# Performance work log

Measured on AMD Instinct MI355X. Metric: run time of the kernel, lower is better.

## Reference

```python
import jax, jax.numpy as jnp
import numpy as np

ALPHA = 0.2
B, D, C = 512, 128, 64


def setup_inputs() -> dict:
    key = jax.random.key(0)
    k1, k2, k3 = jax.random.split(key, 3)
    x = jax.random.normal(k1, (B, D), dtype=jnp.float32)
    x = x / jnp.linalg.norm(x, axis=-1, keepdims=True)  # unit embeddings (2-2*cos distance)
    target = jax.random.randint(k2, (B,), 0, C)
    # uniform noise used for parallel random choice among semi-hard candidates
    noise = jax.random.uniform(k3, (B, B, B), dtype=jnp.float32)
    return {"output": x, "target": target, "noise": noise}


def reference(output, target, noise):
    # pairwise squared euclidean distance for unit-norm embeddings
    d = 2.0 - 2.0 * (output @ output.T)  # [B, B]
    n = d.shape[0]
    same = target[:, None] == target[None, :]          # [B, B] same-label mask
    neg = ~same                                        # [a, n] valid negatives
    pair_mask = same & ~jnp.eye(n, dtype=bool)         # valid (anchor, positive), a != p
    # L[a, p, nn] = d[a, p] - d[a, nn] + alpha
    L = d[:, :, None] - d[:, None, :] + ALPHA          # [B, B, B]
    cand = (L > 0.0) & (L < ALPHA) & neg[:, None, :]   # semi-hard candidate mask
    has_cand = cand.any(axis=-1)                       # [B, B]
    valid = pair_mask & has_cand
    # random choice among candidates: argmax of uniform noise over masked set
    score = jnp.where(cand, noise, -1.0)
    n_idx = jnp.argmax(score, axis=-1)                 # [B, B] chosen negative per pair
    tl = jnp.take_along_axis(L, n_idx[:, :, None], axis=-1)[..., 0]  # triplet loss per pair
    return jnp.where(valid, jnp.maximum(tl, 0.0), 0.0).sum()
```

## Files before the change

### kernel.cpp

```cpp
#include <hip/hip_runtime.h>

#define NB 512
#define ND 128
#define TALPHA 0.2f

__global__ __launch_bounds__(512) void triplet_mine_kernel(
    const float* __restrict__ x,
    const int*   __restrict__ target,
    const float* __restrict__ noise,
    float*       __restrict__ partial)
{
    const int a    = blockIdx.x;
    const int tid  = threadIdx.x;
    const int lane = tid & 63;
    const int wv   = tid >> 6;

    __shared__ __align__(16) float d_row[NB];
    __shared__ __align__(16) int   tgt[NB];
    __shared__ int   plist[NB];
    __shared__ int   pcnt_w[8];
    __shared__ float wacc_s[8];

    const int t_mine = target[tid];
    const int ta     = target[a];
    tgt[tid] = t_mine;

    const bool m = (t_mine == ta) && (tid != a);
    const unsigned long long b = __ballot(m);
    if (lane == 0) pcnt_w[wv] = __popcll(b);
    __syncthreads();

    int base = 0, npos = 0;
    #pragma unroll
    for (int w = 0; w < 8; ++w) {
        base += (w < wv) ? pcnt_w[w] : 0;
        npos += pcnt_w[w];
    }
    if (m) {
        const unsigned long long lower = b & ((1ull << lane) - 1ull);
        plist[base + __popcll(lower)] = tid;
    }
    __syncthreads();

    float4 nv0, nv1;
    if (wv < npos) {
        const int p0 = plist[wv];
        const float* nr = noise + ((size_t)a * NB + (size_t)p0) * NB;
        nv0 = *reinterpret_cast<const float4*>(nr + 4 * lane);
        nv1 = *reinterpret_cast<const float4*>(nr + 256 + 4 * lane);
    }

    const int c    = lane & 3;
    const int rgrp = lane >> 2;
    const float4* xf4 = reinterpret_cast<const float4*>(x);

    float4 xa4[8];
    #pragma unroll
    for (int j = 0; j < 8; ++j) xa4[j] = xf4[(size_t)a * 32 + j * 4 + c];

    #pragma unroll
    for (int q = 0; q < 4; ++q) {
        const int row = q * 128 + wv * 16 + rgrp;
        const float4* rf4 = xf4 + (size_t)row * 32;
        float acc = 0.0f;
        #pragma unroll
        for (int j = 0; j < 8; ++j) {
            const float4 v = rf4[j * 4 + c];
            acc += xa4[j].x * v.x + xa4[j].y * v.y
                 + xa4[j].z * v.z + xa4[j].w * v.w;
        }
        acc += __shfl_xor(acc, 1);
        acc += __shfl_xor(acc, 2);
        if (c == 0) d_row[row] = 2.0f - 2.0f * acc;
    }
    __syncthreads();

    float wacc = 0.0f;
    const float4* d4 = reinterpret_cast<const float4*>(d_row);
    const int4*   t4 = reinterpret_cast<const int4*>(tgt);
    const float4 dd0 = d4[lane];
    const float4 dd1 = d4[64 + lane];
    const int4   tt0 = t4[lane];
    const int4   tt1 = t4[64 + lane];

    for (int idx = wv; idx < npos; idx += 8) {
        float4 nx0, nx1;
        const int nidx = idx + 8;
        if (nidx < npos) {
            const int pn = plist[nidx];
            const float* nr = noise + ((size_t)a * NB + (size_t)pn) * NB;
            nx0 = *reinterpret_cast<const float4*>(nr + 4 * lane);
            nx1 = *reinterpret_cast<const float4*>(nr + 256 + 4 * lane);
        }

        const int p = plist[idx];
        const float d_ap = d_row[p];

        float bs = -1.0f;
        int   bn = NB;

        #define EVAL(nn, dn, tn, sv)                                   \
        {                                                              \
            const float L = d_ap - (dn) + TALPHA;                      \
            if ((L > 0.0f) & (L < TALPHA) & ((tn) != ta)) {            \
                if ((sv) > bs) { bs = (sv); bn = (nn); }               \
            }                                                          \
        }
        EVAL(4*lane + 0,       dd0.x, tt0.x, nv0.x);
        EVAL(4*lane + 1,       dd0.y, tt0.y, nv0.y);
        EVAL(4*lane + 2,       dd0.z, tt0.z, nv0.z);
        EVAL(4*lane + 3,       dd0.w, tt0.w, nv0.w);
        EVAL(256 + 4*lane + 0, dd1.x, tt1.x, nv1.x);
        EVAL(256 + 4*lane + 1, dd1.y, tt1.y, nv1.y);
        EVAL(256 + 4*lane + 2, dd1.z, tt1.z, nv1.z);
        EVAL(256 + 4*lane + 3, dd1.w, tt1.w, nv1.w);
        #undef EVAL

        #pragma unroll
        for (int off = 1; off < 64; off <<= 1) {
            const float os = __shfl_xor(bs, off);
            const int   on = __shfl_xor(bn, off);
            if (os > bs || (os == bs && on < bn)) { bs = os; bn = on; }
        }

        if (bs >= 0.0f) {
            wacc += d_ap - d_row[bn] + TALPHA;
        }

        nv0 = nx0; nv1 = nx1;
    }

    if (lane == 0) wacc_s[wv] = wacc;
    __syncthreads();
    if (tid == 0) {
        float s = 0.0f;
        #pragma unroll
        for (int w = 0; w < 8; ++w) s += wacc_s[w];
        partial[a] = s;
    }
}

__global__ __launch_bounds__(64) void triplet_reduce_kernel(
    const float* __restrict__ partial, float* __restrict__ out)
{
    const int lane = threadIdx.x;
    float s = 0.0f;
    #pragma unroll
    for (int j = 0; j < 8; ++j) s += partial[lane + 64 * j];
    #pragma unroll
    for (int off = 1; off < 64; off <<= 1) s += __shfl_xor(s, off);
    if (lane == 0) out[0] = s;
}

extern "C" void kernel_launch(void* const* d_in, const int* in_sizes, int n_in,
                              void* d_out, int out_size, void* d_ws, size_t ws_size,
                              hipStream_t stream) {
    const float* x      = (const float*)d_in[0];
    const int*   target = (const int*)d_in[1];
    const float* noise  = (const float*)d_in[2];
    float* out     = (float*)d_out;
    float* partial = (float*)d_ws;

    triplet_mine_kernel<<<NB, 512, 0, stream>>>(x, target, noise, partial);
    triplet_reduce_kernel<<<1, 64, 0, stream>>>(partial, out);
}
```

Measured before the change: 15.61 us.

## Process two anchors per block to share x row loads and balance positives

Each block now handles two anchor rows, computing both distance rows from a single pass over x and merging the two positive lists into one tagged work list that the 8 waves share. This halves block count and reuses the loaded x rows for two dot products, and it aims to improve wave utilization when one anchor has few positives. In exchange it adds register pressure (two anchor vectors, two distance rows held in registers) and select logic in the inner loop.

```diff
diff --git a/kernel.cpp b/kernel.cpp
--- a/kernel.cpp
+++ b/kernel.cpp
@@ -10,42 +10,54 @@
     const float* __restrict__ noise,
     float*       __restrict__ partial)
 {
-    const int a    = blockIdx.x;
+    const int a0   = blockIdx.x * 2;
+    const int a1   = a0 + 1;
     const int tid  = threadIdx.x;
     const int lane = tid & 63;
     const int wv   = tid >> 6;
 
-    __shared__ __align__(16) float d_row[NB];
+    __shared__ __align__(16) float d_row[2][NB];
     __shared__ __align__(16) int   tgt[NB];
-    __shared__ int   plist[NB];
-    __shared__ int   pcnt_w[8];
-    __shared__ float wacc_s[8];
+    __shared__ int   plist[2 * NB];
+    __shared__ int   pcnt_w[2][8];
+    __shared__ float wacc_s[8][2];
 
     const int t_mine = target[tid];
-    const int ta     = target[a];
+    const int ta0    = target[a0];
+    const int ta1    = target[a1];
     tgt[tid] = t_mine;
 
-    const bool m = (t_mine == ta) && (tid != a);
-    const unsigned long long b = __ballot(m);
-    if (lane == 0) pcnt_w[wv] = __popcll(b);
+    const bool m0 = (t_mine == ta0) && (tid != a0);
+    const bool m1 = (t_mine == ta1) && (tid != a1);
+    const unsigned long long b0 = __ballot(m0);
+    const unsigned long long b1 = __ballot(m1);
+    if (lane == 0) { pcnt_w[0][wv] = __popcll(b0); pcnt_w[1][wv] = __popcll(b1); }
     __syncthreads();
 
-    int base = 0, npos = 0;
+    int base0 = 0, npos0 = 0, base1 = 0, npos1 = 0;
     #pragma unroll
     for (int w = 0; w < 8; ++w) {
-        base += (w < wv) ? pcnt_w[w] : 0;
-        npos += pcnt_w[w];
+        base0 += (w < wv) ? pcnt_w[0][w] : 0;  npos0 += pcnt_w[0][w];
+        base1 += (w < wv) ? pcnt_w[1][w] : 0;  npos1 += pcnt_w[1][w];
     }
-    if (m) {
-        const unsigned long long lower = b & ((1ull << lane) - 1ull);
-        plist[base + __popcll(lower)] = tid;
+    if (m0) {
+        const unsigned long long lo = b0 & ((1ull << lane) - 1ull);
+        plist[base0 + __popcll(lo)] = tid;
+    }
+    if (m1) {
+        const unsigned long long lo = b1 & ((1ull << lane) - 1ull);
+        plist[npos0 + base1 + __popcll(lo)] = (1 << 16) | tid;
     }
     __syncthreads();
+    const int npos = npos0 + npos1;
 
     float4 nv0, nv1;
+    int ecur = 0;
     if (wv < npos) {
-        const int p0 = plist[wv];
-        const float* nr = noise + ((size_t)a * NB + (size_t)p0) * NB;
+        ecur = plist[wv];
+        const int sel = ecur >> 16;
+        const int p   = ecur & 0xffff;
+        const float* nr = noise + ((size_t)(sel ? a1 : a0) * NB + (size_t)p) * NB;
         nv0 = *reinterpret_cast<const float4*>(nr + 4 * lane);
         nv1 = *reinterpret_cast<const float4*>(nr + 256 + 4 * lane);
     }
@@ -54,47 +66,61 @@
     const int rgrp = lane >> 2;
     const float4* xf4 = reinterpret_cast<const float4*>(x);
 
-    float4 xa4[8];
+    float4 xa0[8], xa1[8];
     #pragma unroll
-    for (int j = 0; j < 8; ++j) xa4[j] = xf4[(size_t)a * 32 + j * 4 + c];
+    for (int j = 0; j < 8; ++j) {
+        xa0[j] = xf4[(size_t)a0 * 32 + j * 4 + c];
+        xa1[j] = xf4[(size_t)a1 * 32 + j * 4 + c];
+    }
 
     #pragma unroll
     for (int q = 0; q < 4; ++q) {
         const int row = q * 128 + wv * 16 + rgrp;
         const float4* rf4 = xf4 + (size_t)row * 32;
-        float acc = 0.0f;
+        float acc0 = 0.0f, acc1 = 0.0f;
         #pragma unroll
         for (int j = 0; j < 8; ++j) {
             const float4 v = rf4[j * 4 + c];
-            acc += xa4[j].x * v.x + xa4[j].y * v.y
-                 + xa4[j].z * v.z + xa4[j].w * v.w;
+            acc0 += xa0[j].x * v.x + xa0[j].y * v.y + xa0[j].z * v.z + xa0[j].w * v.w;
+            acc1 += xa1[j].x * v.x + xa1[j].y * v.y + xa1[j].z * v.z + xa1[j].w * v.w;
         }
-        acc += __shfl_xor(acc, 1);
-        acc += __shfl_xor(acc, 2);
-        if (c == 0) d_row[row] = 2.0f - 2.0f * acc;
+        acc0 += __shfl_xor(acc0, 1);  acc0 += __shfl_xor(acc0, 2);
+        acc1 += __shfl_xor(acc1, 1);  acc1 += __shfl_xor(acc1, 2);
+        if (c == 0) {
+            d_row[0][row] = 2.0f - 2.0f * acc0;
+            d_row[1][row] = 2.0f - 2.0f * acc1;
+        }
     }
     __syncthreads();
 
-    float wacc = 0.0f;
-    const float4* d4 = reinterpret_cast<const float4*>(d_row);
-    const int4*   t4 = reinterpret_cast<const int4*>(tgt);
-    const float4 dd0 = d4[lane];
-    const float4 dd1 = d4[64 + lane];
-    const int4   tt0 = t4[lane];
-    const int4   tt1 = t4[64 + lane];
+    const float4* dA4 = reinterpret_cast<const float4*>(d_row[0]);
+    const float4* dB4 = reinterpret_cast<const float4*>(d_row[1]);
+    const int4*   t4  = reinterpret_cast<const int4*>(tgt);
+    const float4 dA0 = dA4[lane], dA1 = dA4[64 + lane];
+    const float4 dB0 = dB4[lane], dB1 = dB4[64 + lane];
+    const int4   tt0 = t4[lane],  tt1 = t4[64 + lane];
+
+    float wacc0 = 0.0f, wacc1 = 0.0f;
 
     for (int idx = wv; idx < npos; idx += 8) {
         float4 nx0, nx1;
+        int enext = 0;
         const int nidx = idx + 8;
         if (nidx < npos) {
-            const int pn = plist[nidx];
-            const float* nr = noise + ((size_t)a * NB + (size_t)pn) * NB;
+            enext = plist[nidx];
+            const int sn = enext >> 16;
+            const int pn = enext & 0xffff;
+            const float* nr = noise + ((size_t)(sn ? a1 : a0) * NB + (size_t)pn) * NB;
             nx0 = *reinterpret_cast<const float4*>(nr + 4 * lane);
             nx1 = *reinterpret_cast<const float4*>(nr + 256 + 4 * lane);
         }
 
-        const int p = plist[idx];
-        const float d_ap = d_row[p];
+        const int sel = ecur >> 16;
+        const int p   = ecur & 0xffff;
+        const int taS = sel ? ta1 : ta0;
+        const float4 dd0 = sel ? dB0 : dA0;
+        const float4 dd1 = sel ? dB1 : dA1;
+        const float d_ap = sel ? d_row[1][p] : d_row[0][p];
 
         float bs = -1.0f;
         int   bn = NB;
@@ -102,7 +128,7 @@
         #define EVAL(nn, dn, tn, sv)                                   \
         {                                                              \
             const float L = d_ap - (dn) + TALPHA;                      \
-            if ((L > 0.0f) & (L < TALPHA) & ((tn) != ta)) {            \
+            if ((L > 0.0f) & (L < TALPHA) & ((tn) != taS)) {           \
                 if ((sv) > bs) { bs = (sv); bn = (nn); }               \
             }                                                          \
         }
@@ -124,19 +150,21 @@
         }
 
         if (bs >= 0.0f) {
-            wacc += d_ap - d_row[bn] + TALPHA;
+            const float dn = sel ? d_row[1][bn] : d_row[0][bn];
+            const float L  = d_ap - dn + TALPHA;
+            if (sel) wacc1 += L; else wacc0 += L;
         }
 
-        nv0 = nx0; nv1 = nx1;
+        ecur = enext; nv0 = nx0; nv1 = nx1;
     }
 
-    if (lane == 0) wacc_s[wv] = wacc;
+    if (lane == 0) { wacc_s[wv][0] = wacc0; wacc_s[wv][1] = wacc1; }
     __syncthreads();
-    if (tid == 0) {
+    if (tid < 2) {
         float s = 0.0f;
         #pragma unroll
-        for (int w = 0; w < 8; ++w) s += wacc_s[w];
-        partial[a] = s;
+        for (int w = 0; w < 8; ++w) s += wacc_s[w][tid];
+        partial[(tid == 0) ? a0 : a1] = s;
     }
 }
 
@@ -161,6 +189,6 @@
     float* out     = (float*)d_out;
     float* partial = (float*)d_ws;
 
-    triplet_mine_kernel<<<NB, 512, 0, stream>>>(x, target, noise, partial);
+    triplet_mine_kernel<<<NB / 2, 512, 0, stream>>>(x, target, noise, partial);
     triplet_reduce_kernel<<<1, 64, 0, stream>>>(partial, out);
 }
```

New measurement: 16.01 us. 1.03x slower.

## Split distance computation into a tiled GEMM kernel before mining

Applied to the files above, without the earlier changes.

Moves the pairwise distance computation out of the per-anchor mining kernel into a separate shared-memory tiled kernel that writes the full distance matrix to workspace. The mining kernel then reads its distance row from global memory, skips anchors with no positives early, and carries the chosen negative's distance through the wave reduction instead of indexing shared memory. This removes the per-block recomputation of x reads, at the cost of an extra kernel launch and a round-trip of the 1 MB distance matrix through memory.

```diff
diff --git a/kernel.cpp b/kernel.cpp
--- a/kernel.cpp
+++ b/kernel.cpp
@@ -3,9 +3,47 @@
 #define NB 512
 #define ND 128
 #define TALPHA 0.2f
+#define LSTR 132
 
-__global__ __launch_bounds__(512) void triplet_mine_kernel(
+__global__ __launch_bounds__(512) void dist_kernel(
     const float* __restrict__ x,
+    float*       __restrict__ D)
+{
+    const int bx = blockIdx.x, by = blockIdx.y;
+    const int tid = threadIdx.x;
+
+    __shared__ float xr[32 * LSTR];
+    __shared__ float xc[32 * LSTR];
+
+    const float4* xf4 = reinterpret_cast<const float4*>(x);
+    #pragma unroll
+    for (int s = 0; s < 2; ++s) {
+        const int idx = tid + s * 512;
+        const int i = idx >> 5, j = idx & 31;
+        const float4 vr = xf4[((size_t)(by * 32 + i)) * 32 + j];
+        const float4 vc = xf4[((size_t)(bx * 32 + i)) * 32 + j];
+        *reinterpret_cast<float4*>(&xr[i * LSTR + 4 * j]) = vr;
+        *reinterpret_cast<float4*>(&xc[i * LSTR + 4 * j]) = vc;
+    }
+    __syncthreads();
+
+    const int r  = tid >> 4;
+    const int c2 = (tid & 15) * 2;
+    float a0 = 0.0f, a1 = 0.0f;
+    #pragma unroll
+    for (int k = 0; k < ND; k += 4) {
+        const float4 vr = *reinterpret_cast<const float4*>(&xr[r * LSTR + k]);
+        const float4 v0 = *reinterpret_cast<const float4*>(&xc[c2 * LSTR + k]);
+        const float4 v1 = *reinterpret_cast<const float4*>(&xc[(c2 + 1) * LSTR + k]);
+        a0 += vr.x * v0.x + vr.y * v0.y + vr.z * v0.z + vr.w * v0.w;
+        a1 += vr.x * v1.x + vr.y * v1.y + vr.z * v1.z + vr.w * v1.w;
+    }
+    float2 o; o.x = 2.0f - 2.0f * a0; o.y = 2.0f - 2.0f * a1;
+    *reinterpret_cast<float2*>(D + ((size_t)(by * 32 + r)) * NB + bx * 32 + c2) = o;
+}
+
+__global__ __launch_bounds__(512) void mine_kernel(
+    const float* __restrict__ D,
     const int*   __restrict__ target,
     const float* __restrict__ noise,
     float*       __restrict__ partial)
@@ -15,8 +53,7 @@
     const int lane = tid & 63;
     const int wv   = tid >> 6;
 
-    __shared__ __align__(16) float d_row[NB];
-    __shared__ __align__(16) int   tgt[NB];
+    __shared__ __align__(16) int tgt[NB];
     __shared__ int   plist[NB];
     __shared__ int   pcnt_w[8];
     __shared__ float wacc_s[8];
@@ -42,68 +79,45 @@
     }
     __syncthreads();
 
-    float4 nv0, nv1;
+    if (npos == 0) { if (tid == 0) partial[a] = 0.0f; return; }
+
+    const float* Da = D + (size_t)a * NB;
+    const float4 dd0 = *reinterpret_cast<const float4*>(Da + 4 * lane);
+    const float4 dd1 = *reinterpret_cast<const float4*>(Da + 256 + 4 * lane);
+    const int4   tt0 = reinterpret_cast<const int4*>(tgt)[lane];
+    const int4   tt1 = reinterpret_cast<const int4*>(tgt)[64 + lane];
+
+    float4 nv0, nv1; float dap;
     if (wv < npos) {
         const int p0 = plist[wv];
         const float* nr = noise + ((size_t)a * NB + (size_t)p0) * NB;
         nv0 = *reinterpret_cast<const float4*>(nr + 4 * lane);
         nv1 = *reinterpret_cast<const float4*>(nr + 256 + 4 * lane);
+        dap = Da[p0];
     }
 
-    const int c    = lane & 3;
-    const int rgrp = lane >> 2;
-    const float4* xf4 = reinterpret_cast<const float4*>(x);
-
-    float4 xa4[8];
-    #pragma unroll
-    for (int j = 0; j < 8; ++j) xa4[j] = xf4[(size_t)a * 32 + j * 4 + c];
-
-    #pragma unroll
-    for (int q = 0; q < 4; ++q) {
-        const int row = q * 128 + wv * 16 + rgrp;
-        const float4* rf4 = xf4 + (size_t)row * 32;
-        float acc = 0.0f;
-        #pragma unroll
-        for (int j = 0; j < 8; ++j) {
-            const float4 v = rf4[j * 4 + c];
-            acc += xa4[j].x * v.x + xa4[j].y * v.y
-                 + xa4[j].z * v.z + xa4[j].w * v.w;
-        }
-        acc += __shfl_xor(acc, 1);
-        acc += __shfl_xor(acc, 2);
-        if (c == 0) d_row[row] = 2.0f - 2.0f * acc;
-    }
-    __syncthreads();
-
     float wacc = 0.0f;
-    const float4* d4 = reinterpret_cast<const float4*>(d_row);
-    const int4*   t4 = reinterpret_cast<const int4*>(tgt);
-    const float4 dd0 = d4[lane];
-    const float4 dd1 = d4[64 + lane];
-    const int4   tt0 = t4[lane];
-    const int4   tt1 = t4[64 + lane];
 
     for (int idx = wv; idx < npos; idx += 8) {
-        float4 nx0, nx1;
+        float4 nx0, nx1; float dap_n;
         const int nidx = idx + 8;
         if (nidx < npos) {
             const int pn = plist[nidx];
             const float* nr = noise + ((size_t)a * NB + (size_t)pn) * NB;
             nx0 = *reinterpret_cast<const float4*>(nr + 4 * lane);
             nx1 = *reinterpret_cast<const float4*>(nr + 256 + 4 * lane);
+            dap_n = Da[pn];
         }
-
-        const int p = plist[idx];
-        const float d_ap = d_row[p];
 
         float bs = -1.0f;
         int   bn = NB;
+        float bd = 0.0f;
 
         #define EVAL(nn, dn, tn, sv)                                   \
         {                                                              \
-            const float L = d_ap - (dn) + TALPHA;                      \
+            const float L = dap - (dn) + TALPHA;                       \
             if ((L > 0.0f) & (L < TALPHA) & ((tn) != ta)) {            \
-                if ((sv) > bs) { bs = (sv); bn = (nn); }               \
+                if ((sv) > bs) { bs = (sv); bn = (nn); bd = (dn); }    \
             }                                                          \
         }
         EVAL(4*lane + 0,       dd0.x, tt0.x, nv0.x);
@@ -120,14 +134,15 @@
         for (int off = 1; off < 64; off <<= 1) {
             const float os = __shfl_xor(bs, off);
             const int   on = __shfl_xor(bn, off);
-            if (os > bs || (os == bs && on < bn)) { bs = os; bn = on; }
+            const float od = __shfl_xor(bd, off);
+            if (os > bs || (os == bs && on < bn)) { bs = os; bn = on; bd = od; }
         }
 
         if (bs >= 0.0f) {
-            wacc += d_ap - d_row[bn] + TALPHA;
+            wacc += dap - bd + TALPHA;
         }
 
-        nv0 = nx0; nv1 = nx1;
+        nv0 = nx0; nv1 = nx1; dap = dap_n;
     }
 
     if (lane == 0) wacc_s[wv] = wacc;
@@ -140,7 +155,7 @@
     }
 }
 
-__global__ __launch_bounds__(64) void triplet_reduce_kernel(
+__global__ __launch_bounds__(64) void reduce_kernel(
     const float* __restrict__ partial, float* __restrict__ out)
 {
     const int lane = threadIdx.x;
@@ -159,8 +174,10 @@
     const int*   target = (const int*)d_in[1];
     const float* noise  = (const float*)d_in[2];
     float* out     = (float*)d_out;
-    float* partial = (float*)d_ws;
+    float* D       = (float*)d_ws;
+    float* partial = D + (size_t)NB * NB;
 
-    triplet_mine_kernel<<<NB, 512, 0, stream>>>(x, target, noise, partial);
-    triplet_reduce_kernel<<<1, 64, 0, stream>>>(partial, out);
+    dist_kernel<<<dim3(16, 16), 512, 0, stream>>>(x, D);
+    mine_kernel<<<NB, 512, 0, stream>>>(D, target, noise, partial);
+    reduce_kernel<<<1, 64, 0, stream>>>(partial, out);
 }
```

Result: slower. 15.99 us (+2.4%).
